# Performance work log

Measured on AMD Instinct MI355X. Metric: run time of the kernel, lower is better.

Reference implementation:

```python
import jax, jax.numpy as jnp
import numpy as np

THRESHOLD = 0.5

def setup_inputs() -> dict:
    key = jax.random.key(0)
    k1, k2 = jax.random.split(key)
    N, F, B = 800000, 64, 8
    xs = jax.random.uniform(k1, (N, 1), dtype=jnp.float32)          # scores in [0,1)
    pl = jax.random.normal(k2, (N, F), dtype=jnp.float32)           # payload features
    rs = (jnp.arange(B + 1, dtype=jnp.int32) * (N // B))            # row splits [0,100k,...,800k]
    return {"xs": xs, "pl": pl, "rs": rs}

def reference(xs, pl, rs):
    # SelectThreshold(xs, pl, rs, threshold=0.5):
    #   keep rows with score > threshold, compact features, recompute row splits,
    #   and emit scatter indices (original row ids of the kept rows).
    # JIT-static variant: kept rows are stably compacted to the front of an
    # [N, F] buffer; slots >= n_sel are zero-padded, scatter idx padded with N.
    N = pl.shape[0]
    B = rs.shape[0] - 1
    mask = xs[:, 0] > THRESHOLD                                      # [N] bool
    # stable argsort: selected rows first, original (per-segment) order preserved
    order = jnp.argsort(jnp.logical_not(mask))                       # [N] int
    n_sel = jnp.sum(mask.astype(jnp.int32))
    valid = jnp.arange(N) < n_sel                                    # [N] bool
    newfeat = jnp.where(valid[:, None], pl[order], jnp.zeros((), pl.dtype))  # [N, F]
    scatter_idxs = jnp.where(valid, order, N).astype(jnp.int32)[:, None]     # [N, 1]
    # per-event selected counts -> new row splits
    seg_ids = jnp.searchsorted(rs, jnp.arange(N, dtype=rs.dtype), side='right') - 1  # [N]
    counts = jax.ops.segment_sum(mask.astype(rs.dtype), seg_ids, num_segments=B)     # [B]
    new_rs = jnp.concatenate([jnp.zeros((1,), rs.dtype), jnp.cumsum(counts)])        # [B+1]
    return newfeat, new_rs, scatter_idxs
```

## Files before the change

### kernel.cpp

```cpp
#include <hip/hip_runtime.h>


#define THRESH 0.5f
#define RPB 1024

__global__ void k_count(const float* __restrict__ xs, int N,
                        int* __restrict__ ranks, int* __restrict__ blk_counts) {
    __shared__ int wc[4][4];
    const int tid  = threadIdx.x;
    const int lane = tid & 63, wave = tid >> 6;
    const int base = blockIdx.x * RPB;
    int running = 0;
    for (int c = 0; c < 4; ++c) {
        int i = base + c * 256 + tid;
        int m = (i < N) && (xs[i] > THRESH);
        unsigned long long bal = __ballot(m);
        if (lane == 0) wc[c][wave] = __popcll(bal);
        __syncthreads();
        int waveoff = 0, tot = 0;
        for (int w = 0; w < 4; ++w) { int v = wc[c][w]; if (w < wave) waveoff += v; tot += v; }
        int pre = running + waveoff + (int)__popcll(bal & ((1ull << lane) - 1ull));
        if (i < N) ranks[i] = (pre << 1) | m;
        running += tot;
    }
    if (tid == 0) blk_counts[blockIdx.x] = running;
}

__global__ void k_scan(const int* __restrict__ blk_counts, int nblocks,
                       const int* __restrict__ ranks,
                       const int* __restrict__ rs, int nrs, int N,
                       int* __restrict__ blk_off, int* __restrict__ nsel_out,
                       float* __restrict__ out_rs) {
    __shared__ int s[1024];
    __shared__ int s_total;
    const int t = threadIdx.x;
    int v = (t < nblocks) ? blk_counts[t] : 0;
    s[t] = v;
    __syncthreads();
    for (int d = 1; d < 1024; d <<= 1) {
        int add = (t >= d) ? s[t - d] : 0;
        __syncthreads();
        s[t] += add;
        __syncthreads();
    }
    int excl = s[t] - v;
    if (t < nblocks) blk_off[t] = excl;
    if (t == 1023) s_total = s[t];
    __syncthreads();
    int n_sel = s_total;
    if (t == 0) nsel_out[0] = n_sel;
    if (t < nrs) {
        int j = rs[t];
        int val;
        if (j >= N)      val = n_sel;
        else if (j <= 0) val = 0;
        else             val = blk_off[j >> 10] + (ranks[j] >> 1);
        out_rs[t] = (float)val;
    }
}

__global__ void k_scatter(const int* __restrict__ ranks, const int* __restrict__ blk_off,
                          const int* __restrict__ nsel, int N,
                          float* __restrict__ out_sc) {
    int i = blockIdx.x * blockDim.x + threadIdx.x;
    if (i >= N) return;
    int ns = nsel[0];
    int e  = ranks[i];
    if (e & 1) {
        int r = blk_off[i >> 10] + (e >> 1);
        out_sc[r] = (float)i;
    }
    if (i >= ns) out_sc[i] = (float)N;
}

__global__ void k_gather(const float* __restrict__ out_sc, const float4* __restrict__ pl4,
                         int N, float4* __restrict__ outf4) {
    int tid = blockIdx.x * blockDim.x + threadIdx.x;
    int r = tid >> 4;
    int c = tid & 15;
    if (r >= N) return;
    int idx = (int)out_sc[r];
    float4 v = make_float4(0.f, 0.f, 0.f, 0.f);
    if (idx < N) v = pl4[(size_t)idx * 16 + c];
    outf4[(size_t)r * 16 + c] = v;
}

extern "C" void kernel_launch(void* const* d_in, const int* in_sizes, int n_in,
                              void* d_out, int out_size, void* d_ws, size_t ws_size,
                              hipStream_t stream) {
    const float* xs = (const float*)d_in[0];
    const float* pl = (const float*)d_in[1];
    const int*   rs = (const int*)d_in[2];
    const int N   = in_sizes[0];
    const int F   = in_sizes[1] / N;
    const int nrs = in_sizes[2];

    float* out      = (float*)d_out;
    float* out_feat = out;
    float* out_rs   = out + (size_t)N * F;
    float* out_sc   = out_rs + nrs;

    int* ranks      = (int*)d_ws;
    int* blk_counts = ranks + N;
    int* blk_off    = blk_counts + 1024;
    int* nsel       = blk_off + 1024;

    const int nblocks = (N + RPB - 1) / RPB;

    k_count  <<<nblocks,           256,  0, stream>>>(xs, N, ranks, blk_counts);
    k_scan   <<<1,                 1024, 0, stream>>>(blk_counts, nblocks, ranks, rs, nrs, N,
                                                      blk_off, nsel, out_rs);
    k_scatter<<<(N + 255) / 256,   256,  0, stream>>>(ranks, blk_off, nsel, N, out_sc);
    k_gather <<<(N * (F / 4) + 255) / 256, 256, 0, stream>>>(out_sc, (const float4*)pl,
                                                             N, (float4*)out_feat);
}
```

Baseline: 344.6 us.

## Replace per-row rank array with ballot bitmap and fuse scatter/gather into one kernel

The count kernel now stores one 64-bit ballot mask per wave instead of a per-row packed rank, which cuts workspace writes from 4 bytes per row to 1 bit per row. Scatter and gather are merged into a single k_move kernel. Each block rebuilds local prefixes from the bitmap in shared memory, writes scatter indices and copies the selected payload rows directly to their compacted positions. A second half of the grid zero-fills the padding region. This removes the intermediate out_sc read-back and one launch. In exchange, the scan kernel now does a short popcount loop over the bitmap to compute row splits, and some gather work becomes serialised per block.

```diff
diff --git a/kernel.cpp b/kernel.cpp
--- a/kernel.cpp
+++ b/kernel.cpp
@@ -5,34 +5,36 @@
 #define RPB 1024
 
 __global__ void k_count(const float* __restrict__ xs, int N,
-                        int* __restrict__ ranks, int* __restrict__ blk_counts) {
-    __shared__ int wc[4][4];
+                        unsigned long long* __restrict__ bitmap,
+                        int* __restrict__ blk_counts) {
+    __shared__ int wc[16];
     const int tid  = threadIdx.x;
     const int lane = tid & 63, wave = tid >> 6;
     const int base = blockIdx.x * RPB;
-    int running = 0;
     for (int c = 0; c < 4; ++c) {
         int i = base + c * 256 + tid;
         int m = (i < N) && (xs[i] > THRESH);
         unsigned long long bal = __ballot(m);
-        if (lane == 0) wc[c][wave] = __popcll(bal);
-        __syncthreads();
-        int waveoff = 0, tot = 0;
-        for (int w = 0; w < 4; ++w) { int v = wc[c][w]; if (w < wave) waveoff += v; tot += v; }
-        int pre = running + waveoff + (int)__popcll(bal & ((1ull << lane) - 1ull));
-        if (i < N) ranks[i] = (pre << 1) | m;
-        running += tot;
+        if (lane == 0) {
+            int rowstart = base + c * 256 + wave * 64;
+            if (rowstart < N) bitmap[rowstart >> 6] = bal;
+            wc[c * 4 + wave] = __popcll(bal);
+        }
     }
-    if (tid == 0) blk_counts[blockIdx.x] = running;
+    __syncthreads();
+    if (tid == 0) {
+        int s = 0;
+        for (int k = 0; k < 16; ++k) s += wc[k];
+        blk_counts[blockIdx.x] = s;
+    }
 }
 
 __global__ void k_scan(const int* __restrict__ blk_counts, int nblocks,
-                       const int* __restrict__ ranks,
+                       const unsigned long long* __restrict__ bitmap,
                        const int* __restrict__ rs, int nrs, int N,
                        int* __restrict__ blk_off, int* __restrict__ nsel_out,
                        float* __restrict__ out_rs) {
     __shared__ int s[1024];
-    __shared__ int s_total;
     const int t = threadIdx.x;
     int v = (t < nblocks) ? blk_counts[t] : 0;
     s[t] = v;
@@ -43,46 +45,81 @@
         s[t] += add;
         __syncthreads();
     }
-    int excl = s[t] - v;
-    if (t < nblocks) blk_off[t] = excl;
-    if (t == 1023) s_total = s[t];
-    __syncthreads();
-    int n_sel = s_total;
+    int n_sel = s[1023];
+    if (t < nblocks) blk_off[t] = s[t] - v;
     if (t == 0) nsel_out[0] = n_sel;
     if (t < nrs) {
         int j = rs[t];
         int val;
         if (j >= N)      val = n_sel;
         else if (j <= 0) val = 0;
-        else             val = blk_off[j >> 10] + (ranks[j] >> 1);
+        else {
+            int blk = j >> 10;
+            int cnt = (blk == 0) ? 0 : s[blk - 1];
+            for (int w = (blk << 10) >> 6; w < (j >> 6); ++w)
+                cnt += __popcll(bitmap[w]);
+            int rem = j & 63;
+            if (rem) cnt += __popcll(bitmap[j >> 6] & ((1ull << rem) - 1ull));
+            val = cnt;
+        }
         out_rs[t] = (float)val;
     }
 }
 
-__global__ void k_scatter(const int* __restrict__ ranks, const int* __restrict__ blk_off,
-                          const int* __restrict__ nsel, int N,
-                          float* __restrict__ out_sc) {
-    int i = blockIdx.x * blockDim.x + threadIdx.x;
-    if (i >= N) return;
-    int ns = nsel[0];
-    int e  = ranks[i];
-    if (e & 1) {
-        int r = blk_off[i >> 10] + (e >> 1);
-        out_sc[r] = (float)i;
+__global__ void k_move(const float4* __restrict__ pl4,
+                       const unsigned long long* __restrict__ bitmap,
+                       const int* __restrict__ blk_off,
+                       const int* __restrict__ nsel, int N, int nblocks,
+                       float4* __restrict__ outf4, float* __restrict__ out_sc) {
+    const int tid = threadIdx.x;
+    const int b   = blockIdx.x;
+    if (b < nblocks) {
+        __shared__ unsigned long long w[16];
+        __shared__ int wpre[16];
+        __shared__ int rowid[RPB];
+        const int base = b << 10;
+        if (tid < 16) {
+            int rowstart = base + (tid << 6);
+            w[tid] = (rowstart < N) ? bitmap[(base >> 6) + tid] : 0ull;
+        }
+        __syncthreads();
+        if (tid == 0) {
+            int acc = 0;
+            for (int k = 0; k < 16; ++k) { wpre[k] = acc; acc += __popcll(w[k]); }
+        }
+        __syncthreads();
+        const int off = blk_off[b];
+        for (int c = 0; c < 4; ++c) {
+            int r = c * 256 + tid;
+            int i = base + r;
+            int k = r >> 6, bit = r & 63;
+            unsigned long long bw = w[k];
+            if (i < N && ((bw >> bit) & 1ull)) {
+                int pre = wpre[k] + (int)__popcll(bw & ((1ull << bit) - 1ull));
+                rowid[pre] = i;
+                out_sc[off + pre] = (float)i;
+            }
+        }
+        __syncthreads();
+        const int cnt = wpre[15] + (int)__popcll(w[15]);
+        const int cc  = tid & 15;
+        for (int p = tid >> 4; p < cnt; p += 16) {
+            int src = rowid[p];
+            outf4[((size_t)(off + p)) * 16 + cc] = pl4[(size_t)src * 16 + cc];
+        }
+    } else {
+        const int b2    = b - nblocks;
+        const int start = b2 << 10;
+        const int ns    = nsel[0];
+        const int end   = min(start + RPB, N);
+        if (end <= ns) return;
+        const int lo = max(start, ns);
+        for (int s = lo + tid; s < end; s += 256) out_sc[s] = (float)N;
+        const int cc = tid & 15;
+        const float4 z = make_float4(0.f, 0.f, 0.f, 0.f);
+        for (int p = lo + (tid >> 4); p < end; p += 16)
+            outf4[((size_t)p) * 16 + cc] = z;
     }
-    if (i >= ns) out_sc[i] = (float)N;
-}
-
-__global__ void k_gather(const float* __restrict__ out_sc, const float4* __restrict__ pl4,
-                         int N, float4* __restrict__ outf4) {
-    int tid = blockIdx.x * blockDim.x + threadIdx.x;
-    int r = tid >> 4;
-    int c = tid & 15;
-    if (r >= N) return;
-    int idx = (int)out_sc[r];
-    float4 v = make_float4(0.f, 0.f, 0.f, 0.f);
-    if (idx < N) v = pl4[(size_t)idx * 16 + c];
-    outf4[(size_t)r * 16 + c] = v;
 }
 
 extern "C" void kernel_launch(void* const* d_in, const int* in_sizes, int n_in,
@@ -100,17 +137,17 @@
     float* out_rs   = out + (size_t)N * F;
     float* out_sc   = out_rs + nrs;
 
-    int* ranks      = (int*)d_ws;
-    int* blk_counts = ranks + N;
+    const int nwords = (N + 63) / 64;
+    unsigned long long* bitmap = (unsigned long long*)d_ws;
+    int* blk_counts = (int*)(bitmap + nwords);
     int* blk_off    = blk_counts + 1024;
     int* nsel       = blk_off + 1024;
 
     const int nblocks = (N + RPB - 1) / RPB;
 
-    k_count  <<<nblocks,           256,  0, stream>>>(xs, N, ranks, blk_counts);
-    k_scan   <<<1,                 1024, 0, stream>>>(blk_counts, nblocks, ranks, rs, nrs, N,
-                                                      blk_off, nsel, out_rs);
-    k_scatter<<<(N + 255) / 256,   256,  0, stream>>>(ranks, blk_off, nsel, N, out_sc);
-    k_gather <<<(N * (F / 4) + 255) / 256, 256, 0, stream>>>(out_sc, (const float4*)pl,
-                                                             N, (float4*)out_feat);
+    k_count<<<nblocks,     256,  0, stream>>>(xs, N, bitmap, blk_counts);
+    k_scan <<<1,           1024, 0, stream>>>(blk_counts, nblocks, bitmap, rs, nrs, N,
+                                              blk_off, nsel, out_rs);
+    k_move <<<2 * nblocks, 256,  0, stream>>>((const float4*)pl, bitmap, blk_off, nsel,
+                                              N, nblocks, (float4*)out_feat, out_sc);
 }
```

Result: slower. 366.2 us (+6.3%).
